# Kernel tuning notes

Measured on AMD Instinct MI355X. Metric: run time of the kernel, lower is better.

## Reference

```python
import jax, jax.numpy as jnp
import numpy as np

IN_Q = 256   # in_features // 4
OUT_Q = 256  # out_features // 4


def setup_inputs() -> dict:
    key = jax.random.key(0)
    kx, kr, ki, kj, kk = jax.random.split(key, 5)
    stdv = 1.0 / np.sqrt(IN_Q)
    return {
        "x": jax.random.normal(kx, (4, 8192, IN_Q * 4), dtype=jnp.float32),
        "r_weight": jax.random.uniform(kr, (OUT_Q, IN_Q), minval=-stdv, maxval=stdv, dtype=jnp.float32),
        "i_weight": jax.random.uniform(ki, (OUT_Q, IN_Q), minval=-stdv, maxval=stdv, dtype=jnp.float32),
        "j_weight": jax.random.uniform(kj, (OUT_Q, IN_Q), minval=-stdv, maxval=stdv, dtype=jnp.float32),
        "k_weight": jax.random.uniform(kk, (OUT_Q, IN_Q), minval=-stdv, maxval=stdv, dtype=jnp.float32),
        "bias": jnp.zeros((OUT_Q * 4,), dtype=jnp.float32),
    }


def reference(x, r_weight, i_weight, j_weight, k_weight, bias):
    batch_dims = x.shape[:-1]
    xq = x.reshape(*batch_dims, IN_Q, 4)  # [..., in_q, 4]
    r_x, i_x, j_x, k_x = xq[..., 0], xq[..., 1], xq[..., 2], xq[..., 3]

    lin = lambda v, w: jnp.einsum('...i,oi->...o', v, w)  # F.linear, no bias

    out_r = lin(r_x, r_weight) - lin(i_x, i_weight) - lin(j_x, j_weight) - lin(k_x, k_weight)
    out_i = lin(r_x, i_weight) + lin(i_x, r_weight) + lin(j_x, k_weight) - lin(k_x, j_weight)
    out_j = lin(r_x, j_weight) - lin(i_x, k_weight) + lin(j_x, r_weight) + lin(k_x, i_weight)
    out_k = lin(r_x, k_weight) + lin(i_x, j_weight) - lin(j_x, i_weight) + lin(k_x, r_weight)

    out = jnp.stack([out_r, out_i, out_j, out_k], axis=-1)  # [..., out_q, 4]
    out = out.reshape(*batch_dims, OUT_Q * 4)
    return out + bias
```

## Files before the change

### kernel.cpp

```cpp
#include <hip/hip_runtime.h>


typedef __attribute__((ext_vector_type(8))) short bf16x8;
typedef __attribute__((ext_vector_type(16))) float f32x16;

#define M_TOT 32768
#define N_TOT 1024
#define K_TOT 1024
#define BM 256
#define BN 256
#define BK 64
#define NKT (K_TOT / BK)

__device__ __forceinline__ unsigned short f2bf(float f) {
    union { float f; unsigned int u; } v; v.f = f;
    unsigned int u = v.u;
    u += 0x7fffu + ((u >> 16) & 1u);
    return (unsigned short)(u >> 16);
}

__device__ __forceinline__ unsigned int pk2(float lo, float hi) {
    unsigned int r;
    asm("v_cvt_pk_bf16_f32 %0, %1, %2" : "=v"(r) : "v"(lo), "v"(hi));
    return r;
}

__device__ __forceinline__ bf16x8 cvt8(float4 a, float4 b) {
    union { unsigned int u[4]; bf16x8 v; } r;
    r.u[0] = pk2(a.x, a.y); r.u[1] = pk2(a.z, a.w);
    r.u[2] = pk2(b.x, b.y); r.u[3] = pk2(b.z, b.w);
    return r.v;
}

__global__ __launch_bounds__(256) void build_w(const float* __restrict__ R,
                                               const float* __restrict__ I,
                                               const float* __restrict__ J,
                                               const float* __restrict__ Kw,
                                               ushort4* __restrict__ Wb) {
    int n = blockIdx.x;
    int i = threadIdx.x;
    int o = n >> 2, co = n & 3;
    int base = o * 256 + i;
    float r = R[base], ii = I[base], j = J[base], k = Kw[base];
    float v0, v1, v2, v3;
    if (co == 0)      { v0 = r;  v1 = -ii; v2 = -j;  v3 = -k; }
    else if (co == 1) { v0 = ii; v1 = r;   v2 = k;   v3 = -j; }
    else if (co == 2) { v0 = j;  v1 = -k;  v2 = r;   v3 = ii; }
    else              { v0 = k;  v1 = j;   v2 = -ii; v3 = r;  }
    ushort4 w;
    w.x = f2bf(v0); w.y = f2bf(v1); w.z = f2bf(v2); w.w = f2bf(v3);
    Wb[n * 256 + i] = w;
}

__device__ __forceinline__ void async_lds16(const void* g, void* l) {
    __builtin_amdgcn_global_load_lds(
        (const __attribute__((address_space(1))) unsigned int*)g,
        (__attribute__((address_space(3))) unsigned int*)l,
        16, 0, 0);
}

__device__ __forceinline__ void stage_ht(const unsigned short* __restrict__ G,
                                         int row0, int k0,
                                         unsigned short* ht,
                                         int wave, int lane) {
    int sr = lane >> 2;
    int sc = ((lane & 3) * 8) ^ ((lane & 32) ? 16 : 0)
           ^ (((wave >> 1) & 1) ? 24 : 0);
#pragma unroll
    for (int j = 0; j < 2; ++j) {
        int si = j * 8 + wave;
        int rg = si >> 1, cg = si & 1;
        async_lds16(G + (size_t)(row0 + rg * 16 + sr) * K_TOT + k0 + cg * 32 + sc,
                    ht + si * 512);
    }
}

__global__ __launch_bounds__(512, 2) void gemm_fused(
        const float* __restrict__ X,
        const unsigned short* __restrict__ B,
        const float* __restrict__ bias,
        float* __restrict__ C) {
    __shared__ unsigned short smemA[2][2][8192];
    __shared__ unsigned short smemB[2][2][8192];

    const int tid  = threadIdx.x;
    const int wave = tid >> 6;
    const int lane = tid & 63;
    const int wm   = wave & 1;
    const int wn   = wave >> 1;

    int bid = blockIdx.x;
    int wg  = (bid & 7) * 64 + (bid >> 3);
    const int m0 = (wg >> 2) * BM;
    const int n0 = (wg & 3) * BN;

    const int laneRd = (lane & 15) * 32
                     + ((lane >> 4) & 1) * 1024;
    const int klo8 = ((lane >> 5) & 1) << 3;
    const int rxor = ((lane & 8) << 1)
                   ^ (((lane >> 4) & 1) ? 24 : 0);
    const int kofs[2] = { klo8 ^ rxor, (klo8 ^ rxor) ^ 16 };
    const unsigned short* baseA = &smemA[0][wm][0] + laneRd;
    const unsigned short* baseB = &smemB[0][wn >> 1][0] + (wn & 1) * 4096 + laneRd;

    const int srow = (lane >> 2) & 15;
    const int skc  = lane & 3;
    unsigned short* wbase = &smemA[0][0][0] + wave * 512 + srow * 32
                          + ((skc * 8) ^ ((lane & 32) ? 16 : 0)
                                       ^ (((wave >> 1) & 1) ? 24 : 0));
    const float* gBase = X + (size_t)(m0 + (wave >> 1) * 16 + srow) * K_TOT
                       + (wave & 1) * 32 + skc * 8;

    f32x16 acc[4][2];
#pragma unroll
    for (int i = 0; i < 4; ++i)
#pragma unroll
        for (int j = 0; j < 2; ++j)
#pragma unroll
            for (int r = 0; r < 16; ++r)
                acc[i][j][r] = 0.f;

    float4 aq0a, aq0b, aq1a, aq1b;
    float4 bq0a, bq0b, bq1a, bq1b;

    stage_ht(B, n0,       0, &smemB[0][0][0], wave, lane);
    stage_ht(B, n0 + 128, 0, &smemB[0][1][0], wave, lane);
#pragma unroll
    for (int tt = 0; tt < 2; ++tt)
#pragma unroll
        for (int rh = 0; rh < 2; ++rh)
#pragma unroll
            for (int h = 0; h < 2; ++h) {
                const float* g = gBase + (size_t)h * 131072 + rh * 65536 + tt * BK;
                float4 a = *(const float4*)g;
                float4 b = *(const float4*)(g + 4);
                *(bf16x8*)(wbase + tt * 16384 + h * 8192 + rh * 4096) = cvt8(a, b);
            }
    aq0a = *(const float4*)(gBase + 2 * BK);
    aq0b = *(const float4*)(gBase + 2 * BK + 4);
    aq1a = *(const float4*)(gBase + 131072 + 2 * BK);
    aq1b = *(const float4*)(gBase + 131072 + 2 * BK + 4);
    asm volatile("s_waitcnt vmcnt(4)" ::: "memory");
    asm volatile("s_waitcnt lgkmcnt(0)" ::: "memory");
    __builtin_amdgcn_s_barrier();

    bf16x8 af[2][4], bl[4], bh[4];

#pragma unroll 2
    for (int t = 0; t < NKT; ++t) {
        const int c  = t & 1;
        const int cA = c * 16384;

#pragma unroll
        for (int rb = 0; rb < 2; ++rb)
#pragma unroll
            for (int ks = 0; ks < 4; ++ks)
                af[rb][ks] = *(const bf16x8*)(baseA + cA + rb * 2048
                                              + (ks >> 1) * 512 + kofs[ks & 1]);
#pragma unroll
        for (int ks = 0; ks < 4; ++ks)
            bl[ks] = *(const bf16x8*)(baseB + cA + (ks >> 1) * 512 + kofs[ks & 1]);
        if (t + 2 < NKT) {
            const int k2 = (t + 2) * BK;
            bq0a = *(const float4*)(gBase + 65536 + k2);
            bq0b = *(const float4*)(gBase + 65536 + k2 + 4);
            bq1a = *(const float4*)(gBase + 131072 + 65536 + k2);
            bq1b = *(const float4*)(gBase + 131072 + 65536 + k2 + 4);
        }
        if (t + 1 < NKT) {
            stage_ht(B, n0,       (t + 1) * BK, &smemB[c ^ 1][0][0], wave, lane);
            stage_ht(B, n0 + 128, (t + 1) * BK, &smemB[c ^ 1][1][0], wave, lane);
        }
        __builtin_amdgcn_s_barrier();
        asm volatile("s_waitcnt lgkmcnt(0)" ::: "memory");
        __builtin_amdgcn_s_setprio(1);
#pragma unroll
        for (int rb = 0; rb < 2; ++rb)
#pragma unroll
            for (int ks = 0; ks < 4; ++ks)
                acc[rb][0] = __builtin_amdgcn_mfma_f32_32x32x16_bf16(
                    af[rb][ks], bl[ks], acc[rb][0], 0, 0, 0);
        __builtin_amdgcn_s_setprio(0);
        __builtin_amdgcn_s_barrier();

#pragma unroll
        for (int ks = 0; ks < 4; ++ks)
            bh[ks] = *(const bf16x8*)(baseB + cA + 2048
                                      + (ks >> 1) * 512 + kofs[ks & 1]);
        if (t + 2 < NKT) {
            *(bf16x8*)(wbase + cA)        = cvt8(aq0a, aq0b);
            *(bf16x8*)(wbase + cA + 8192) = cvt8(aq1a, aq1b);
        }
        __builtin_amdgcn_s_barrier();
        asm volatile("s_waitcnt lgkmcnt(0)" ::: "memory");
        __builtin_amdgcn_s_setprio(1);
#pragma unroll
        for (int rb = 0; rb < 2; ++rb)
#pragma unroll
            for (int ks = 0; ks < 4; ++ks)
                acc[rb][1] = __builtin_amdgcn_mfma_f32_32x32x16_bf16(
                    af[rb][ks], bh[ks], acc[rb][1], 0, 0, 0);
        __builtin_amdgcn_s_setprio(0);
        __builtin_amdgcn_s_barrier();

#pragma unroll
        for (int rb = 0; rb < 2; ++rb)
#pragma unroll
            for (int ks = 0; ks < 4; ++ks)
                af[rb][ks] = *(const bf16x8*)(baseA + cA + (rb + 2) * 2048
                                              + (ks >> 1) * 512 + kofs[ks & 1]);
        if (t + 3 < NKT) {
            const int k3 = (t + 3) * BK;
            aq0a = *(const float4*)(gBase + k3);
            aq0b = *(const float4*)(gBase + k3 + 4);
            aq1a = *(const float4*)(gBase + 131072 + k3);
            aq1b = *(const float4*)(gBase + 131072 + k3 + 4);
        }
        __builtin_amdgcn_s_barrier();
        asm volatile("s_waitcnt lgkmcnt(0)" ::: "memory");
        __builtin_amdgcn_s_setprio(1);
#pragma unroll
        for (int rb = 0; rb < 2; ++rb)
#pragma unroll
            for (int ks = 0; ks < 4; ++ks)
                acc[rb + 2][1] = __builtin_amdgcn_mfma_f32_32x32x16_bf16(
                    af[rb][ks], bh[ks], acc[rb + 2][1], 0, 0, 0);
        __builtin_amdgcn_s_setprio(0);
        __builtin_amdgcn_s_barrier();

        __builtin_amdgcn_s_setprio(1);
#pragma unroll
        for (int rb = 0; rb < 2; ++rb)
#pragma unroll
            for (int ks = 0; ks < 4; ++ks)
                acc[rb + 2][0] = __builtin_amdgcn_mfma_f32_32x32x16_bf16(
                    af[rb][ks], bl[ks], acc[rb + 2][0], 0, 0, 0);
        __builtin_amdgcn_s_setprio(0);
        if (t + 2 < NKT) {
            *(bf16x8*)(wbase + cA + 4096)        = cvt8(bq0a, bq0b);
            *(bf16x8*)(wbase + cA + 8192 + 4096) = cvt8(bq1a, bq1b);
        }
        if (t + 3 < NKT) {
            asm volatile("s_waitcnt vmcnt(4)" ::: "memory");
        } else if (t + 1 < NKT) {
            asm volatile("s_waitcnt vmcnt(0)" ::: "memory");
        }
        asm volatile("s_waitcnt lgkmcnt(0)" ::: "memory");
        __builtin_amdgcn_s_barrier();
    }

    const int mbase = m0 + wm * 128 + ((lane >> 5) & 1) * 4;
    const int nbase = n0 + wn * 64 + (lane & 31);
#pragma unroll
    for (int cb = 0; cb < 2; ++cb) {
        int col  = nbase + cb * 32;
        float bv = bias[col];
#pragma unroll
        for (int rb = 0; rb < 4; ++rb) {
            f32x16 v = acc[rb][cb];
#pragma unroll
            for (int r = 0; r < 16; ++r) {
                int row = mbase + rb * 32 + (r & 3) + (r >> 2) * 8;
                C[(size_t)row * N_TOT + col] = v[r] + bv;
            }
        }
    }
}

extern "C" void kernel_launch(void* const* d_in, const int* in_sizes, int n_in,
                              void* d_out, int out_size, void* d_ws, size_t ws_size,
                              hipStream_t stream) {
    const float* x    = (const float*)d_in[0];
    const float* rw   = (const float*)d_in[1];
    const float* iw   = (const float*)d_in[2];
    const float* jw   = (const float*)d_in[3];
    const float* kw   = (const float*)d_in[4];
    const float* bias = (const float*)d_in[5];
    float* out = (float*)d_out;

    unsigned short* Wb = (unsigned short*)d_ws;

    build_w<<<N_TOT, 256, 0, stream>>>(rw, iw, jw, kw, (ushort4*)Wb);

    gemm_fused<<<dim3((M_TOT / BM) * (N_TOT / BN)), 512, 0, stream>>>(
        x, Wb, bias, out);
}
```

Baseline: 300.2 us.

## Switch main GEMM from 32x32x16 to 16x16x32 MFMA with new LDS swizzle

Replaces the 32x32x16 bf16 MFMA tiling with 16x16x32 MFMAs, so each wave now holds an 8x4 grid of 4-float accumulators. The LDS swizzle for A/B staging and fragment reads is simplified to a single XOR pattern. Global-load prefetches and bf16 conversion stores are reordered across the phases, and the vmcnt wait condition changes. This aims for a cheaper read-address pattern and different MFMA issue behaviour. The risks are more LDS bank conflicts, lower per-instruction MFMA efficiency, and altered pipeline timing.

```diff
diff --git a/kernel.cpp b/kernel.cpp
--- a/kernel.cpp
+++ b/kernel.cpp
@@ -2,7 +2,7 @@
 
 
 typedef __attribute__((ext_vector_type(8))) short bf16x8;
-typedef __attribute__((ext_vector_type(16))) float f32x16;
+typedef __attribute__((ext_vector_type(4))) float f32x4;
 
 #define M_TOT 32768
 #define N_TOT 1024
@@ -64,8 +64,7 @@
                                          unsigned short* ht,
                                          int wave, int lane) {
     int sr = lane >> 2;
-    int sc = ((lane & 3) * 8) ^ ((lane & 32) ? 16 : 0)
-           ^ (((wave >> 1) & 1) ? 24 : 0);
+    int sc = ((lane & 3) * 8) ^ ((lane & 32) ? 16 : 0);
 #pragma unroll
     for (int j = 0; j < 2; ++j) {
         int si = j * 8 + wave;
@@ -86,6 +85,8 @@
     const int tid  = threadIdx.x;
     const int wave = tid >> 6;
     const int lane = tid & 63;
+    const int quad = lane >> 4;
+    const int r16  = lane & 15;
     const int wm   = wave & 1;
     const int wn   = wave >> 1;
 
@@ -94,31 +95,23 @@
     const int m0 = (wg >> 2) * BM;
     const int n0 = (wg & 3) * BN;
 
-    const int laneRd = (lane & 15) * 32
-                     + ((lane >> 4) & 1) * 1024;
-    const int klo8 = ((lane >> 5) & 1) << 3;
-    const int rxor = ((lane & 8) << 1)
-                   ^ (((lane >> 4) & 1) ? 24 : 0);
-    const int kofs[2] = { klo8 ^ rxor, (klo8 ^ rxor) ^ 16 };
+    const int laneRd = (r16 * 32 + quad * 8) ^ ((r16 & 8) << 1);
     const unsigned short* baseA = &smemA[0][wm][0] + laneRd;
     const unsigned short* baseB = &smemB[0][wn >> 1][0] + (wn & 1) * 4096 + laneRd;
 
     const int srow = (lane >> 2) & 15;
     const int skc  = lane & 3;
     unsigned short* wbase = &smemA[0][0][0] + wave * 512 + srow * 32
-                          + ((skc * 8) ^ ((lane & 32) ? 16 : 0)
-                                       ^ (((wave >> 1) & 1) ? 24 : 0));
+                          + ((skc * 8) ^ ((lane & 32) ? 16 : 0));
     const float* gBase = X + (size_t)(m0 + (wave >> 1) * 16 + srow) * K_TOT
                        + (wave & 1) * 32 + skc * 8;
 
-    f32x16 acc[4][2];
-#pragma unroll
-    for (int i = 0; i < 4; ++i)
-#pragma unroll
-        for (int j = 0; j < 2; ++j)
-#pragma unroll
-            for (int r = 0; r < 16; ++r)
-                acc[i][j][r] = 0.f;
+    f32x4 acc[8][4];
+#pragma unroll
+    for (int i = 0; i < 8; ++i)
+#pragma unroll
+        for (int j = 0; j < 4; ++j)
+            acc[i][j] = (f32x4){0.f, 0.f, 0.f, 0.f};
 
     float4 aq0a, aq0b, aq1a, aq1b;
     float4 bq0a, bq0b, bq1a, bq1b;
@@ -144,7 +137,7 @@
     asm volatile("s_waitcnt lgkmcnt(0)" ::: "memory");
     __builtin_amdgcn_s_barrier();
 
-    bf16x8 af[2][4], bl[4], bh[4];
+    bf16x8 af[4][2], bl[2][2], bh[2][2];
 
 #pragma unroll 2
     for (int t = 0; t < NKT; ++t) {
@@ -152,63 +145,70 @@
         const int cA = c * 16384;
 
 #pragma unroll
-        for (int rb = 0; rb < 2; ++rb)
-#pragma unroll
-            for (int ks = 0; ks < 4; ++ks)
-                af[rb][ks] = *(const bf16x8*)(baseA + cA + rb * 2048
-                                              + (ks >> 1) * 512 + kofs[ks & 1]);
-#pragma unroll
-        for (int ks = 0; ks < 4; ++ks)
-            bl[ks] = *(const bf16x8*)(baseB + cA + (ks >> 1) * 512 + kofs[ks & 1]);
+        for (int mb = 0; mb < 4; ++mb)
+#pragma unroll
+            for (int ks = 0; ks < 2; ++ks)
+                af[mb][ks] = *(const bf16x8*)(baseA + cA + (mb * 2 + ks) * 512);
+#pragma unroll
+        for (int nb = 0; nb < 2; ++nb)
+#pragma unroll
+            for (int ks = 0; ks < 2; ++ks)
+                bl[nb][ks] = *(const bf16x8*)(baseB + cA + (nb * 2 + ks) * 512);
+        if (t + 1 < NKT) {
+            stage_ht(B, n0,       (t + 1) * BK, &smemB[c ^ 1][0][0], wave, lane);
+            stage_ht(B, n0 + 128, (t + 1) * BK, &smemB[c ^ 1][1][0], wave, lane);
+        }
+        __builtin_amdgcn_s_barrier();
+        asm volatile("s_waitcnt lgkmcnt(0)" ::: "memory");
+        __builtin_amdgcn_s_setprio(1);
+#pragma unroll
+        for (int mb = 0; mb < 4; ++mb)
+#pragma unroll
+            for (int nb = 0; nb < 2; ++nb) {
+                acc[mb][nb] = __builtin_amdgcn_mfma_f32_16x16x32_bf16(
+                    af[mb][0], bl[nb][0], acc[mb][nb], 0, 0, 0);
+                acc[mb][nb] = __builtin_amdgcn_mfma_f32_16x16x32_bf16(
+                    af[mb][1], bl[nb][1], acc[mb][nb], 0, 0, 0);
+            }
+        __builtin_amdgcn_s_setprio(0);
+        __builtin_amdgcn_s_barrier();
+
+#pragma unroll
+        for (int nb = 0; nb < 2; ++nb)
+#pragma unroll
+            for (int ks = 0; ks < 2; ++ks)
+                bh[nb][ks] = *(const bf16x8*)(baseB + cA
+                                              + ((nb + 2) * 2 + ks) * 512);
         if (t + 2 < NKT) {
             const int k2 = (t + 2) * BK;
+            *(bf16x8*)(wbase + cA)        = cvt8(aq0a, aq0b);
+            *(bf16x8*)(wbase + cA + 8192) = cvt8(aq1a, aq1b);
             bq0a = *(const float4*)(gBase + 65536 + k2);
             bq0b = *(const float4*)(gBase + 65536 + k2 + 4);
             bq1a = *(const float4*)(gBase + 131072 + 65536 + k2);
             bq1b = *(const float4*)(gBase + 131072 + 65536 + k2 + 4);
         }
-        if (t + 1 < NKT) {
-            stage_ht(B, n0,       (t + 1) * BK, &smemB[c ^ 1][0][0], wave, lane);
-            stage_ht(B, n0 + 128, (t + 1) * BK, &smemB[c ^ 1][1][0], wave, lane);
-        }
-        __builtin_amdgcn_s_barrier();
-        asm volatile("s_waitcnt lgkmcnt(0)" ::: "memory");
-        __builtin_amdgcn_s_setprio(1);
-#pragma unroll
-        for (int rb = 0; rb < 2; ++rb)
-#pragma unroll
-            for (int ks = 0; ks < 4; ++ks)
-                acc[rb][0] = __builtin_amdgcn_mfma_f32_32x32x16_bf16(
-                    af[rb][ks], bl[ks], acc[rb][0], 0, 0, 0);
-        __builtin_amdgcn_s_setprio(0);
-        __builtin_amdgcn_s_barrier();
-
-#pragma unroll
-        for (int ks = 0; ks < 4; ++ks)
-            bh[ks] = *(const bf16x8*)(baseB + cA + 2048
-                                      + (ks >> 1) * 512 + kofs[ks & 1]);
-        if (t + 2 < NKT) {
-            *(bf16x8*)(wbase + cA)        = cvt8(aq0a, aq0b);
-            *(bf16x8*)(wbase + cA + 8192) = cvt8(aq1a, aq1b);
-        }
-        __builtin_amdgcn_s_barrier();
-        asm volatile("s_waitcnt lgkmcnt(0)" ::: "memory");
-        __builtin_amdgcn_s_setprio(1);
-#pragma unroll
-        for (int rb = 0; rb < 2; ++rb)
-#pragma unroll
-            for (int ks = 0; ks < 4; ++ks)
-                acc[rb][1] = __builtin_amdgcn_mfma_f32_32x32x16_bf16(
-                    af[rb][ks], bh[ks], acc[rb][1], 0, 0, 0);
-        __builtin_amdgcn_s_setprio(0);
-        __builtin_amdgcn_s_barrier();
-
-#pragma unroll
-        for (int rb = 0; rb < 2; ++rb)
-#pragma unroll
-            for (int ks = 0; ks < 4; ++ks)
-                af[rb][ks] = *(const bf16x8*)(baseA + cA + (rb + 2) * 2048
-                                              + (ks >> 1) * 512 + kofs[ks & 1]);
+        __builtin_amdgcn_s_barrier();
+        asm volatile("s_waitcnt lgkmcnt(0)" ::: "memory");
+        __builtin_amdgcn_s_setprio(1);
+#pragma unroll
+        for (int mb = 0; mb < 4; ++mb)
+#pragma unroll
+            for (int nb = 0; nb < 2; ++nb) {
+                acc[mb][nb + 2] = __builtin_amdgcn_mfma_f32_16x16x32_bf16(
+                    af[mb][0], bh[nb][0], acc[mb][nb + 2], 0, 0, 0);
+                acc[mb][nb + 2] = __builtin_amdgcn_mfma_f32_16x16x32_bf16(
+                    af[mb][1], bh[nb][1], acc[mb][nb + 2], 0, 0, 0);
+            }
+        __builtin_amdgcn_s_setprio(0);
+        __builtin_amdgcn_s_barrier();
+
+#pragma unroll
+        for (int mb = 0; mb < 4; ++mb)
+#pragma unroll
+            for (int ks = 0; ks < 2; ++ks)
+                af[mb][ks] = *(const bf16x8*)(baseA + cA
+                                              + ((mb + 4) * 2 + ks) * 512);
         if (t + 3 < NKT) {
             const int k3 = (t + 3) * BK;
             aq0a = *(const float4*)(gBase + k3);
@@ -220,27 +220,33 @@
         asm volatile("s_waitcnt lgkmcnt(0)" ::: "memory");
         __builtin_amdgcn_s_setprio(1);
 #pragma unroll
-        for (int rb = 0; rb < 2; ++rb)
-#pragma unroll
-            for (int ks = 0; ks < 4; ++ks)
-                acc[rb + 2][1] = __builtin_amdgcn_mfma_f32_32x32x16_bf16(
-                    af[rb][ks], bh[ks], acc[rb + 2][1], 0, 0, 0);
-        __builtin_amdgcn_s_setprio(0);
-        __builtin_amdgcn_s_barrier();
-
-        __builtin_amdgcn_s_setprio(1);
-#pragma unroll
-        for (int rb = 0; rb < 2; ++rb)
-#pragma unroll
-            for (int ks = 0; ks < 4; ++ks)
-                acc[rb + 2][0] = __builtin_amdgcn_mfma_f32_32x32x16_bf16(
-                    af[rb][ks], bl[ks], acc[rb + 2][0], 0, 0, 0);
+        for (int mb = 0; mb < 4; ++mb)
+#pragma unroll
+            for (int nb = 0; nb < 2; ++nb) {
+                acc[mb + 4][nb + 2] = __builtin_amdgcn_mfma_f32_16x16x32_bf16(
+                    af[mb][0], bh[nb][0], acc[mb + 4][nb + 2], 0, 0, 0);
+                acc[mb + 4][nb + 2] = __builtin_amdgcn_mfma_f32_16x16x32_bf16(
+                    af[mb][1], bh[nb][1], acc[mb + 4][nb + 2], 0, 0, 0);
+            }
+        __builtin_amdgcn_s_setprio(0);
+        __builtin_amdgcn_s_barrier();
+
+        __builtin_amdgcn_s_setprio(1);
+#pragma unroll
+        for (int mb = 0; mb < 4; ++mb)
+#pragma unroll
+            for (int nb = 0; nb < 2; ++nb) {
+                acc[mb + 4][nb] = __builtin_amdgcn_mfma_f32_16x16x32_bf16(
+                    af[mb][0], bl[nb][0], acc[mb + 4][nb], 0, 0, 0);
+                acc[mb + 4][nb] = __builtin_amdgcn_mfma_f32_16x16x32_bf16(
+                    af[mb][1], bl[nb][1], acc[mb + 4][nb], 0, 0, 0);
+            }
         __builtin_amdgcn_s_setprio(0);
         if (t + 2 < NKT) {
             *(bf16x8*)(wbase + cA + 4096)        = cvt8(bq0a, bq0b);
             *(bf16x8*)(wbase + cA + 8192 + 4096) = cvt8(bq1a, bq1b);
         }
-        if (t + 3 < NKT) {
+        if (t + 2 < NKT) {
             asm volatile("s_waitcnt vmcnt(4)" ::: "memory");
         } else if (t + 1 < NKT) {
             asm volatile("s_waitcnt vmcnt(0)" ::: "memory");
@@ -249,20 +255,19 @@
         __builtin_amdgcn_s_barrier();
     }
 
-    const int mbase = m0 + wm * 128 + ((lane >> 5) & 1) * 4;
-    const int nbase = n0 + wn * 64 + (lane & 31);
-#pragma unroll
-    for (int cb = 0; cb < 2; ++cb) {
-        int col  = nbase + cb * 32;
+    const int mbase = m0 + wm * 128 + quad * 4;
+    const int nbase = n0 + wn * 64 + r16;
+#pragma unroll
+    for (int nb = 0; nb < 4; ++nb) {
+        int col  = nbase + nb * 16;
         float bv = bias[col];
 #pragma unroll
-        for (int rb = 0; rb < 4; ++rb) {
-            f32x16 v = acc[rb][cb];
-#pragma unroll
-            for (int r = 0; r < 16; ++r) {
-                int row = mbase + rb * 32 + (r & 3) + (r >> 2) * 8;
-                C[(size_t)row * N_TOT + col] = v[r] + bv;
-            }
+        for (int mb = 0; mb < 8; ++mb) {
+            int rowb = mbase + mb * 16;
+            f32x4 v  = acc[mb][nb];
+#pragma unroll
+            for (int r = 0; r < 4; ++r)
+                C[(size_t)(rowb + r) * N_TOT + col] = v[r] + bv;
         }
     }
 }
```

Result: slower. 310.8 us (+3.5%).

## Make each workgroup compute two M tiles with continuous cross-tile pipelining

Applied to the files above, without the earlier changes.

The grid is halved to 256 workgroups. Each workgroup now processes two output tiles 16384 rows apart, so the K-loop runs twice as long and global prefetch of the second tile's X overlaps the first tile's tail compute. The first tile's results are stored mid-loop and the accumulators are reset, removing pipeline prologue and epilogue bubbles between tiles. The trade-off is fewer workgroups, which may underfill the CUs, and a store burst that lands in the middle of the loop.

```diff
diff --git a/kernel.cpp b/kernel.cpp
--- a/kernel.cpp
+++ b/kernel.cpp
@@ -11,6 +11,8 @@
 #define BN 256
 #define BK 64
 #define NKT (K_TOT / BK)
+#define TT_TOT (2 * NKT)
+#define POFF ((size_t)16384 * 1024)
 
 __device__ __forceinline__ unsigned short f2bf(float f) {
     union { float f; unsigned int u; } v; v.f = f;
@@ -90,9 +92,10 @@
     const int wn   = wave >> 1;
 
     int bid = blockIdx.x;
-    int wg  = (bid & 7) * 64 + (bid >> 3);
-    const int m0 = (wg >> 2) * BM;
-    const int n0 = (wg & 3) * BN;
+    int wg  = (bid & 7) * 32 + (bid >> 3);
+    const int mg  = wg >> 2;
+    const int n0  = (wg & 3) * BN;
+    const size_t m0row = (size_t)mg * BM;
 
     const int laneRd = (lane & 15) * 32
                      + ((lane >> 4) & 1) * 1024;
@@ -108,8 +111,9 @@
     unsigned short* wbase = &smemA[0][0][0] + wave * 512 + srow * 32
                           + ((skc * 8) ^ ((lane & 32) ? 16 : 0)
                                        ^ (((wave >> 1) & 1) ? 24 : 0));
-    const float* gBase = X + (size_t)(m0 + (wave >> 1) * 16 + srow) * K_TOT
-                       + (wave & 1) * 32 + skc * 8;
+    const float* gB0 = X + (m0row + (wave >> 1) * 16 + srow) * K_TOT
+                     + (wave & 1) * 32 + skc * 8;
+    const float* gB1 = gB0 + POFF;
 
     f32x16 acc[4][2];
 #pragma unroll
@@ -126,20 +130,20 @@
     stage_ht(B, n0,       0, &smemB[0][0][0], wave, lane);
     stage_ht(B, n0 + 128, 0, &smemB[0][1][0], wave, lane);
 #pragma unroll
-    for (int tt = 0; tt < 2; ++tt)
+    for (int ttp = 0; ttp < 2; ++ttp)
 #pragma unroll
         for (int rh = 0; rh < 2; ++rh)
 #pragma unroll
             for (int h = 0; h < 2; ++h) {
-                const float* g = gBase + (size_t)h * 131072 + rh * 65536 + tt * BK;
+                const float* g = gB0 + (size_t)h * 131072 + rh * 65536 + ttp * BK;
                 float4 a = *(const float4*)g;
                 float4 b = *(const float4*)(g + 4);
-                *(bf16x8*)(wbase + tt * 16384 + h * 8192 + rh * 4096) = cvt8(a, b);
+                *(bf16x8*)(wbase + ttp * 16384 + h * 8192 + rh * 4096) = cvt8(a, b);
             }
-    aq0a = *(const float4*)(gBase + 2 * BK);
-    aq0b = *(const float4*)(gBase + 2 * BK + 4);
-    aq1a = *(const float4*)(gBase + 131072 + 2 * BK);
-    aq1b = *(const float4*)(gBase + 131072 + 2 * BK + 4);
+    aq0a = *(const float4*)(gB0 + 2 * BK);
+    aq0b = *(const float4*)(gB0 + 2 * BK + 4);
+    aq1a = *(const float4*)(gB0 + 131072 + 2 * BK);
+    aq1b = *(const float4*)(gB0 + 131072 + 2 * BK + 4);
     asm volatile("s_waitcnt vmcnt(4)" ::: "memory");
     asm volatile("s_waitcnt lgkmcnt(0)" ::: "memory");
     __builtin_amdgcn_s_barrier();
@@ -147,8 +151,8 @@
     bf16x8 af[2][4], bl[4], bh[4];
 
 #pragma unroll 2
-    for (int t = 0; t < NKT; ++t) {
-        const int c  = t & 1;
+    for (int tt = 0; tt < TT_TOT; ++tt) {
+        const int c  = tt & 1;
         const int cA = c * 16384;
 
 #pragma unroll
@@ -160,16 +164,10 @@
 #pragma unroll
         for (int ks = 0; ks < 4; ++ks)
             bl[ks] = *(const bf16x8*)(baseB + cA + (ks >> 1) * 512 + kofs[ks & 1]);
-        if (t + 2 < NKT) {
-            const int k2 = (t + 2) * BK;
-            bq0a = *(const float4*)(gBase + 65536 + k2);
-            bq0b = *(const float4*)(gBase + 65536 + k2 + 4);
-            bq1a = *(const float4*)(gBase + 131072 + 65536 + k2);
-            bq1b = *(const float4*)(gBase + 131072 + 65536 + k2 + 4);
-        }
-        if (t + 1 < NKT) {
-            stage_ht(B, n0,       (t + 1) * BK, &smemB[c ^ 1][0][0], wave, lane);
-            stage_ht(B, n0 + 128, (t + 1) * BK, &smemB[c ^ 1][1][0], wave, lane);
+        if (tt + 1 < TT_TOT) {
+            const int ku = ((tt + 1) & (NKT - 1)) * BK;
+            stage_ht(B, n0,       ku, &smemB[c ^ 1][0][0], wave, lane);
+            stage_ht(B, n0 + 128, ku, &smemB[c ^ 1][1][0], wave, lane);
         }
         __builtin_amdgcn_s_barrier();
         asm volatile("s_waitcnt lgkmcnt(0)" ::: "memory");
@@ -187,9 +185,16 @@
         for (int ks = 0; ks < 4; ++ks)
             bh[ks] = *(const bf16x8*)(baseB + cA + 2048
                                       + (ks >> 1) * 512 + kofs[ks & 1]);
-        if (t + 2 < NKT) {
+        if (tt + 2 < TT_TOT) {
+            const int u  = tt + 2;
+            const float* gb = (u >= NKT) ? gB1 : gB0;
+            const int k2 = (u & (NKT - 1)) * BK;
             *(bf16x8*)(wbase + cA)        = cvt8(aq0a, aq0b);
             *(bf16x8*)(wbase + cA + 8192) = cvt8(aq1a, aq1b);
+            bq0a = *(const float4*)(gb + 65536 + k2);
+            bq0b = *(const float4*)(gb + 65536 + k2 + 4);
+            bq1a = *(const float4*)(gb + 131072 + 65536 + k2);
+            bq1b = *(const float4*)(gb + 131072 + 65536 + k2 + 4);
         }
         __builtin_amdgcn_s_barrier();
         asm volatile("s_waitcnt lgkmcnt(0)" ::: "memory");
@@ -209,12 +214,14 @@
             for (int ks = 0; ks < 4; ++ks)
                 af[rb][ks] = *(const bf16x8*)(baseA + cA + (rb + 2) * 2048
                                               + (ks >> 1) * 512 + kofs[ks & 1]);
-        if (t + 3 < NKT) {
-            const int k3 = (t + 3) * BK;
-            aq0a = *(const float4*)(gBase + k3);
-            aq0b = *(const float4*)(gBase + k3 + 4);
-            aq1a = *(const float4*)(gBase + 131072 + k3);
-            aq1b = *(const float4*)(gBase + 131072 + k3 + 4);
+        if (tt + 3 < TT_TOT) {
+            const int u  = tt + 3;
+            const float* gb = (u >= NKT) ? gB1 : gB0;
+            const int k3 = (u & (NKT - 1)) * BK;
+            aq0a = *(const float4*)(gb + k3);
+            aq0b = *(const float4*)(gb + k3 + 4);
+            aq1a = *(const float4*)(gb + 131072 + k3);
+            aq1b = *(const float4*)(gb + 131072 + k3 + 4);
         }
         __builtin_amdgcn_s_barrier();
         asm volatile("s_waitcnt lgkmcnt(0)" ::: "memory");
@@ -236,31 +243,57 @@
                 acc[rb + 2][0] = __builtin_amdgcn_mfma_f32_32x32x16_bf16(
                     af[rb][ks], bl[ks], acc[rb + 2][0], 0, 0, 0);
         __builtin_amdgcn_s_setprio(0);
-        if (t + 2 < NKT) {
+        if (tt + 2 < TT_TOT) {
             *(bf16x8*)(wbase + cA + 4096)        = cvt8(bq0a, bq0b);
             *(bf16x8*)(wbase + cA + 8192 + 4096) = cvt8(bq1a, bq1b);
         }
-        if (t + 3 < NKT) {
+        if (tt + 3 < TT_TOT) {
             asm volatile("s_waitcnt vmcnt(4)" ::: "memory");
-        } else if (t + 1 < NKT) {
+        } else if (tt + 1 < TT_TOT) {
             asm volatile("s_waitcnt vmcnt(0)" ::: "memory");
         }
         asm volatile("s_waitcnt lgkmcnt(0)" ::: "memory");
         __builtin_amdgcn_s_barrier();
+
+        if (tt == NKT - 1) {
+            const int mb0 = (int)m0row + wm * 128 + ((lane >> 5) & 1) * 4;
+            const int nb0 = n0 + wn * 64 + (lane & 31);
+#pragma unroll
+            for (int cb = 0; cb < 2; ++cb) {
+                int col  = nb0 + cb * 32;
+                float bv = bias[col];
+#pragma unroll
+                for (int rb = 0; rb < 4; ++rb) {
+                    f32x16 v = acc[rb][cb];
+#pragma unroll
+                    for (int r = 0; r < 16; ++r) {
+                        int row = mb0 + rb * 32 + (r & 3) + (r >> 2) * 8;
+                        C[(size_t)row * N_TOT + col] = v[r] + bv;
+                    }
+                }
+            }
+#pragma unroll
+            for (int i = 0; i < 4; ++i)
+#pragma unroll
+                for (int j = 0; j < 2; ++j)
+#pragma unroll
+                    for (int r = 0; r < 16; ++r)
+                        acc[i][j][r] = 0.f;
+        }
     }
 
-    const int mbase = m0 + wm * 128 + ((lane >> 5) & 1) * 4;
-    const int nbase = n0 + wn * 64 + (lane & 31);
+    const int mb1 = (int)m0row + 16384 + wm * 128 + ((lane >> 5) & 1) * 4;
+    const int nb1 = n0 + wn * 64 + (lane & 31);
 #pragma unroll
     for (int cb = 0; cb < 2; ++cb) {
-        int col  = nbase + cb * 32;
+        int col  = nb1 + cb * 32;
         float bv = bias[col];
 #pragma unroll
         for (int rb = 0; rb < 4; ++rb) {
             f32x16 v = acc[rb][cb];
 #pragma unroll
             for (int r = 0; r < 16; ++r) {
-                int row = mbase + rb * 32 + (r & 3) + (r >> 2) * 8;
+                int row = mb1 + rb * 32 + (r & 3) + (r >> 2) * 8;
                 C[(size_t)row * N_TOT + col] = v[r] + bv;
             }
         }
@@ -282,6 +315,5 @@
 
     build_w<<<N_TOT, 256, 0, stream>>>(rw, iw, jw, kw, (ushort4*)Wb);
 
-    gemm_fused<<<dim3((M_TOT / BM) * (N_TOT / BN)), 512, 0, stream>>>(
-        x, Wb, bias, out);
-}
+    gemm_fused<<<dim3(256), 512, 0, stream>>>(x, Wb, bias, out);
+}
```

New measurement: 311.1 us. 1.04x slower.
